# Performance work log

Measured on AMD Instinct MI355X. Metric: run time of the kernel, lower is better.

## Reference

```python
import jax, jax.numpy as jnp
import numpy as np

B, D, N, H, K = 8192, 1024, 4096, 8, 4
T, DECAY, STEPS = 100.0, 0.001, 3


def setup_inputs() -> dict:
    key = jax.random.key(0)
    ks = jax.random.split(key, 16)
    rn = lambda k, sh, s=0.02: jax.random.normal(k, sh, jnp.float32) * s
    return {
        'query': jax.random.normal(ks[0], (B, D), jnp.float32),
        'wm': jax.random.normal(ks[1], (B, D), jnp.float32),
        'keys': jax.random.normal(ks[2], (N, D), jnp.float32) * 0.1,
        'values': jax.random.normal(ks[3], (N, D), jnp.float32) * 0.1,
        'last_access': jax.random.uniform(ks[4], (N,), jnp.float32) * T,
        'importance': jnp.ones((N,), jnp.float32),
        'consolid': jnp.ones((N,), jnp.float32),
        'emo_tags': jax.random.uniform(ks[5], (N, 8), jnp.float32),
        'active': jnp.ones((N,), jnp.float32),
        'in_proj_w': rn(ks[6], (3 * D, D)), 'in_proj_b': jnp.zeros((3 * D,), jnp.float32),
        'out_w': rn(ks[7], (D, D)), 'out_b': jnp.zeros((D,), jnp.float32),
        'msg_w1': rn(ks[8], (D, 2 * D)), 'msg_b1': jnp.zeros((D,), jnp.float32),
        'msg_ln_g': jnp.ones((D,), jnp.float32), 'msg_ln_b': jnp.zeros((D,), jnp.float32),
        'msg_w2': rn(ks[9], (D, D)), 'msg_b2': jnp.zeros((D,), jnp.float32),
        'gru_wih': rn(ks[10], (3 * D, D)), 'gru_whh': rn(ks[11], (3 * D, D)),
        'gru_bih': jnp.zeros((3 * D,), jnp.float32), 'gru_bhh': jnp.zeros((3 * D,), jnp.float32),
        'rsn_w1': rn(ks[12], (D, D)), 'rsn_b1': jnp.zeros((D,), jnp.float32),
        'rsn_ln_g': jnp.ones((D,), jnp.float32), 'rsn_ln_b': jnp.zeros((D,), jnp.float32),
        'rsn_w2': rn(ks[13], (D, D)), 'rsn_b2': jnp.zeros((D,), jnp.float32),
        'top_k': K,
    }


def _ln(x, g, b):
    m = x.mean(-1, keepdims=True)
    v = ((x - m) ** 2).mean(-1, keepdims=True)
    return (x - m) / jnp.sqrt(v + 1e-5) * g + b


def reference(query, wm, keys, values, last_access, importance, consolid, emo_tags, active,
              in_proj_w, in_proj_b, out_w, out_b,
              msg_w1, msg_b1, msg_ln_g, msg_ln_b, msg_w2, msg_b2,
              gru_wih, gru_whh, gru_bih, gru_bhh,
              rsn_w1, rsn_b1, rsn_ln_g, rsn_ln_b, rsn_w2, rsn_b2, top_k):
    sg = jax.lax.stop_gradient
    # --- schema retrieve: cosine sim + forgetting-decay + boosts + topk softmax gather ---
    qn = query / jnp.maximum(jnp.linalg.norm(query, axis=-1, keepdims=True), 1e-8)
    kn = keys / jnp.maximum(jnp.linalg.norm(keys, axis=-1, keepdims=True), 1e-8)
    sims = qn @ kn.T  # [B, N]
    forget = sg(jnp.exp(-DECAY * (T - last_access)))
    boost = sg(emo_tags.sum(-1) * 0.1 + importance * 0.2 + jnp.log1p(consolid) * 0.1)
    scores = (sims * forget + boost) * sg(active)
    top_s, top_i = jax.lax.top_k(scores, top_k)  # [B, K]
    w = jax.nn.softmax(top_s, axis=-1)
    schema = jnp.einsum('bk,bkd->bd', w, values[top_i])  # [B, D]

    # --- GraphReasoner: 3 steps of 2-token MHA + msg_net + GRUCell ---
    dh = D // H
    scale = 1.0 / np.sqrt(dh).astype(np.float32)

    def mha(x):  # x [B, 2, D]
        qkv = x @ in_proj_w.T + in_proj_b
        q, k, v = jnp.split(qkv, 3, axis=-1)
        q = q.reshape(-1, 2, H, dh); k = k.reshape(-1, 2, H, dh); v = v.reshape(-1, 2, H, dh)
        a = jax.nn.softmax(jnp.einsum('bqhd,bkhd->bhqk', q, k) * scale, axis=-1)
        o = jnp.einsum('bhqk,bkhd->bqhd', a, v).reshape(-1, 2, D)
        return o @ out_w.T + out_b

    def gru(x, h):
        gi = x @ gru_wih.T + gru_bih
        gh = h @ gru_whh.T + gru_bhh
        ir, iz, inn = jnp.split(gi, 3, axis=-1)
        hr, hz, hn = jnp.split(gh, 3, axis=-1)
        r = jax.nn.sigmoid(ir + hr)
        z = jax.nn.sigmoid(iz + hz)
        n = jnp.tanh(inn + r * hn)
        return (1.0 - z) * n + z * h

    state = wm
    for _ in range(STEPS):
        ctx = jnp.stack([state, schema], axis=1)  # [B, 2, D]
        att = mha(ctx)
        combined = jnp.concatenate([att[:, 0], att[:, 1]], axis=-1)  # [B, 2D]
        msg = jax.nn.relu(_ln(combined @ msg_w1.T + msg_b1, msg_ln_g, msg_ln_b)) @ msg_w2.T + msg_b2
        state = gru(msg, state)
    out = jax.nn.relu(_ln(state @ rsn_w1.T + rsn_b1, rsn_ln_g, rsn_ln_b)) @ rsn_w2.T + rsn_b2
    return out
```

## Files before the change

kernel.cpp:

```cpp
#include <hip/hip_runtime.h>
#include <cstdint>
#include <cstddef>

typedef __attribute__((ext_vector_type(8))) short short8;
typedef __attribute__((ext_vector_type(4))) float f32x4;
typedef __attribute__((ext_vector_type(4))) unsigned short us4;

#define DEVINL static __device__ __forceinline__

DEVINL float bf2f(unsigned short u){
  union { unsigned uu; float f; } v; v.uu = ((unsigned)u) << 16; return v.f;
}
DEVINL unsigned short f2bf(float f){
  unsigned u = __float_as_uint(f);
  u += 0x7fffu + ((u >> 16) & 1u);
  return (unsigned short)(u >> 16);
}

DEVINL bool tk_better(float av, int ai, float bv, int bi){
  return (av > bv) || (av == bv && ai < bi);
}
DEVINL void tk_cmpex(float& va, int& ia, float& vb, int& ib){
  if (!tk_better(va, ia, vb, ib)){
    float tv = va; va = vb; vb = tv;
    int t = ia; ia = ib; ib = t;
  }
}
DEVINL void tk_sort4(float* v, int* id){
  tk_cmpex(v[0], id[0], v[1], id[1]);
  tk_cmpex(v[2], id[2], v[3], id[3]);
  tk_cmpex(v[0], id[0], v[2], id[2]);
  tk_cmpex(v[1], id[1], v[3], id[3]);
  tk_cmpex(v[1], id[1], v[2], id[2]);
}
DEVINL void tk_bmerge(float* v, int* id, const float* pv, const int* pi){
  #pragma unroll
  for (int i = 0; i < 4; ++i){
    bool ta = tk_better(v[i], id[i], pv[3 - i], pi[3 - i]);
    v[i]  = ta ? v[i]  : pv[3 - i];
    id[i] = ta ? id[i] : pi[3 - i];
  }
  tk_cmpex(v[0], id[0], v[2], id[2]);
  tk_cmpex(v[1], id[1], v[3], id[3]);
  tk_cmpex(v[0], id[0], v[1], id[1]);
  tk_cmpex(v[2], id[2], v[3], id[3]);
}

__global__ void k_diag(float* out, float v){ out[0] = v; }

__global__ __launch_bounds__(256) void k_cast_bf16(const float* __restrict__ x,
                                                   unsigned short* __restrict__ y, int n4){
  int stride = gridDim.x * blockDim.x;
  for (int i = blockIdx.x * blockDim.x + threadIdx.x; i < n4; i += stride){
    float4 v = ((const float4*)x)[i];
    us4 o; o[0] = f2bf(v.x); o[1] = f2bf(v.y); o[2] = f2bf(v.z); o[3] = f2bf(v.w);
    ((us4*)y)[i] = o;
  }
}

__global__ __launch_bounds__(256) void k_prep_keys(const float* __restrict__ keys,
    const float* __restrict__ last_access, const float* __restrict__ importance,
    const float* __restrict__ consolid, const float* __restrict__ emo,
    const float* __restrict__ active, float* __restrict__ ascale, float* __restrict__ bbias){
  int wave = threadIdx.x >> 6, lane = threadIdx.x & 63;
  int n = blockIdx.x * 4 + wave;
  const float* kr = keys + (size_t)n * 1024;
  float s = 0.f;
  #pragma unroll
  for (int j = 0; j < 4; ++j){
    float4 v = ((const float4*)kr)[j * 64 + lane];
    s += v.x*v.x + v.y*v.y + v.z*v.z + v.w*v.w;
  }
  #pragma unroll
  for (int m = 32; m >= 1; m >>= 1) s += __shfl_xor(s, m);
  if (lane == 0){
    float norm = fmaxf(sqrtf(s), 1e-8f);
    float forget = expf(-0.001f * (100.0f - last_access[n]));
    float bo = 0.f;
    #pragma unroll
    for (int j = 0; j < 8; ++j) bo += emo[n * 8 + j];
    bo = bo * 0.1f + importance[n] * 0.2f + log1pf(consolid[n]) * 0.1f;
    float a = active[n];
    ascale[n] = forget * a / norm;
    bbias[n]  = bo * a;
  }
}

__global__ __launch_bounds__(256) void k_qnorm(const float* __restrict__ q, float* __restrict__ qinv){
  int wave = threadIdx.x >> 6, lane = threadIdx.x & 63;
  int b = blockIdx.x * 4 + wave;
  const float* qr = q + (size_t)b * 1024;
  float s = 0.f;
  #pragma unroll
  for (int j = 0; j < 4; ++j){
    float4 v = ((const float4*)qr)[j * 64 + lane];
    s += v.x*v.x + v.y*v.y + v.z*v.z + v.w*v.w;
  }
  #pragma unroll
  for (int m = 32; m >= 1; m >>= 1) s += __shfl_xor(s, m);
  if (lane == 0) qinv[b] = 1.0f / fmaxf(sqrtf(s), 1e-8f);
}

__global__ __launch_bounds__(256) void k_split(const float* __restrict__ X,
    const float* __restrict__ rscale, unsigned short* __restrict__ Hi,
    unsigned short* __restrict__ Lo){
  const int row = blockIdx.x;
  const float sc = rscale ? rscale[row] : 1.0f;
  const int d = threadIdx.x * 4;
  float4 v = *(const float4*)(X + (size_t)row * 1024 + d);
  float xs[4] = {v.x * sc, v.y * sc, v.z * sc, v.w * sc};
  us4 h, l;
  #pragma unroll
  for (int j = 0; j < 4; ++j){
    unsigned short hb = f2bf(xs[j]);
    h[j] = hb;
    l[j] = f2bf(xs[j] - bf2f(hb));
  }
  *(us4*)(Hi + (size_t)row * 1024 + d) = h;
  *(us4*)(Lo + (size_t)row * 1024 + d) = l;
}

__global__ __launch_bounds__(256) void k_scores_mfma(
    const unsigned short* __restrict__ Qhi, const unsigned short* __restrict__ Qlo,
    const unsigned short* __restrict__ Khi, const unsigned short* __restrict__ Klo,
    const float* __restrict__ ascale, const float* __restrict__ bbias,
    float* __restrict__ candV, int* __restrict__ candI){
  __shared__ __align__(16) unsigned short AsH[128 * 32];
  __shared__ __align__(16) unsigned short AsL[128 * 32];
  __shared__ __align__(16) unsigned short BsH[128 * 32];
  __shared__ __align__(16) unsigned short BsL[128 * 32];
  const int tid = threadIdx.x;
  const int wave = tid >> 6, lane = tid & 63;
  const int tM = blockIdx.x, tN = blockIdx.y;
  const int wm_ = wave >> 1, wn_ = wave & 1;
  f32x4 acc[4][4] = {};
  const unsigned short* AH = Qhi + (size_t)tM * 128 * 1024;
  const unsigned short* AL = Qlo + (size_t)tM * 128 * 1024;
  const unsigned short* BH = Khi + (size_t)tN * 128 * 1024;
  const unsigned short* BL = Klo + (size_t)tN * 128 * 1024;
  const int lrow = lane & 15, lk = (lane >> 4) * 8;
  for (int k0 = 0; k0 < 1024; k0 += 32){
    __syncthreads();
    #pragma unroll
    for (int j = 0; j < 2; ++j){
      int c = wave * 128 + j * 64 + lane;
      int row = c >> 2, cp = c & 3;
      size_t go = (size_t)row * 1024 + k0 + cp * 8;
      int lo_ = (wave * 2 + j) * 512;
      __builtin_amdgcn_global_load_lds((const __attribute__((address_space(1))) void*)(AH + go),
          (__attribute__((address_space(3))) void*)(AsH + lo_), 16, 0, 0);
      __builtin_amdgcn_global_load_lds((const __attribute__((address_space(1))) void*)(AL + go),
          (__attribute__((address_space(3))) void*)(AsL + lo_), 16, 0, 0);
      __builtin_amdgcn_global_load_lds((const __attribute__((address_space(1))) void*)(BH + go),
          (__attribute__((address_space(3))) void*)(BsH + lo_), 16, 0, 0);
      __builtin_amdgcn_global_load_lds((const __attribute__((address_space(1))) void*)(BL + go),
          (__attribute__((address_space(3))) void*)(BsL + lo_), 16, 0, 0);
    }
    __syncthreads();
    short8 ah[4], al[4], bh[4], bl[4];
    #pragma unroll
    for (int mi = 0; mi < 4; ++mi){
      int ro = (wm_ * 64 + mi * 16 + lrow) * 32 + lk;
      ah[mi] = *(const short8*)(AsH + ro);
      al[mi] = *(const short8*)(AsL + ro);
    }
    #pragma unroll
    for (int ni = 0; ni < 4; ++ni){
      int ro = (wn_ * 64 + ni * 16 + lrow) * 32 + lk;
      bh[ni] = *(const short8*)(BsH + ro);
      bl[ni] = *(const short8*)(BsL + ro);
    }
    #pragma unroll
    for (int mi = 0; mi < 4; ++mi)
      #pragma unroll
      for (int ni = 0; ni < 4; ++ni){
        acc[mi][ni] = __builtin_amdgcn_mfma_f32_16x16x32_bf16(ah[mi], bh[ni], acc[mi][ni], 0, 0, 0);
        acc[mi][ni] = __builtin_amdgcn_mfma_f32_16x16x32_bf16(ah[mi], bl[ni], acc[mi][ni], 0, 0, 0);
        acc[mi][ni] = __builtin_amdgcn_mfma_f32_16x16x32_bf16(al[mi], bh[ni], acc[mi][ni], 0, 0, 0);
      }
  }
  const int lc = lane & 15;
  float as_[4], bb_[4]; int cid[4];
  #pragma unroll
  for (int ni = 0; ni < 4; ++ni){
    cid[ni] = tN * 128 + wn_ * 64 + ni * 16 + lc;
    as_[ni] = ascale[cid[ni]];
    bb_[ni] = bbias[cid[ni]];
  }
  #pragma unroll
  for (int mi = 0; mi < 4; ++mi){
    #pragma unroll
    for (int r = 0; r < 4; ++r){
      float v[4]; int id[4];
      #pragma unroll
      for (int ni = 0; ni < 4; ++ni){
        v[ni]  = acc[mi][ni][r] * as_[ni] + bb_[ni];
        id[ni] = cid[ni];
      }
      tk_sort4(v, id);
      #pragma unroll
      for (int mask = 1; mask <= 8; mask <<= 1){
        float pv[4]; int pi_[4];
        #pragma unroll
        for (int j = 0; j < 4; ++j){
          pv[j]  = __shfl_xor(v[j], mask);
          pi_[j] = __shfl_xor(id[j], mask);
        }
        tk_bmerge(v, id, pv, pi_);
      }
      if (lc == 0){
        int row = tM * 128 + wm_ * 64 + mi * 16 + (lane >> 4) * 4 + r;
        size_t cb = (size_t)row * 256 + tN * 8 + wn_ * 4;
        #pragma unroll
        for (int j = 0; j < 4; ++j){ candV[cb + j] = v[j]; candI[cb + j] = id[j]; }
      }
    }
  }
}

__global__ __launch_bounds__(256) void k_topk_merge(const float* __restrict__ candV,
    const int* __restrict__ candI, const float* __restrict__ V,
    unsigned short* __restrict__ schema_bf){
  const int row = blockIdx.x, tid = threadIdx.x;
  const int wave = tid >> 6, lane = tid & 63;
  float v[4]; int id[4];
  v[0] = candV[(size_t)row * 256 + tid];
  id[0] = candI[(size_t)row * 256 + tid];
  #pragma unroll
  for (int j = 1; j < 4; ++j){ v[j] = -3.4e38f; id[j] = 0x7fffffff; }
  #pragma unroll
  for (int mask = 1; mask <= 32; mask <<= 1){
    float pv[4]; int pi_[4];
    #pragma unroll
    for (int j = 0; j < 4; ++j){
      pv[j]  = __shfl_xor(v[j], mask);
      pi_[j] = __shfl_xor(id[j], mask);
    }
    tk_bmerge(v, id, pv, pi_);
  }
  __shared__ float wv[4][4]; __shared__ int wi[4][4];
  if (lane == 0){
    #pragma unroll
    for (int j = 0; j < 4; ++j){ wv[wave][j] = v[j]; wi[wave][j] = id[j]; }
  }
  __syncthreads();
  __shared__ float w_sh[4]; __shared__ int i_sh[4];
  if (tid == 0){
    float fv[4]; int fi[4];
    #pragma unroll
    for (int j = 0; j < 4; ++j){ fv[j] = wv[0][j]; fi[j] = wi[0][j]; }
    #pragma unroll
    for (int w = 1; w < 4; ++w){
      float pv[4]; int pi_[4];
      #pragma unroll
      for (int j = 0; j < 4; ++j){ pv[j] = wv[w][j]; pi_[j] = wi[w][j]; }
      tk_bmerge(fv, fi, pv, pi_);
    }
    float m = fv[0];
    float e0 = expf(fv[0] - m), e1 = expf(fv[1] - m), e2 = expf(fv[2] - m), e3 = expf(fv[3] - m);
    float inv = 1.f / (e0 + e1 + e2 + e3);
    w_sh[0] = e0 * inv; w_sh[1] = e1 * inv; w_sh[2] = e2 * inv; w_sh[3] = e3 * inv;
    i_sh[0] = fi[0]; i_sh[1] = fi[1]; i_sh[2] = fi[2]; i_sh[3] = fi[3];
  }
  __syncthreads();
  float w0 = w_sh[0], w1 = w_sh[1], w2 = w_sh[2], w3 = w_sh[3];
  const float* v0 = V + (size_t)i_sh[0] * 1024;
  const float* v1 = V + (size_t)i_sh[1] * 1024;
  const float* v2 = V + (size_t)i_sh[2] * 1024;
  const float* v3 = V + (size_t)i_sh[3] * 1024;
  int d = tid * 4;
  float4 a = *(const float4*)(v0 + d);
  float4 b4 = *(const float4*)(v1 + d);
  float4 c = *(const float4*)(v2 + d);
  float4 e = *(const float4*)(v3 + d);
  us4 o;
  o[0] = f2bf(w0*a.x + w1*b4.x + w2*c.x + w3*e.x);
  o[1] = f2bf(w0*a.y + w1*b4.y + w2*c.y + w3*e.y);
  o[2] = f2bf(w0*a.z + w1*b4.z + w2*c.z + w3*e.z);
  o[3] = f2bf(w0*a.w + w1*b4.w + w2*c.w + w3*e.w);
  *(us4*)(schema_bf + (size_t)row * 1024 + d) = o;
}

__global__ __launch_bounds__(256) void k_initstate(const float* __restrict__ wm,
    float* __restrict__ st, unsigned short* __restrict__ stbf){
  size_t i = ((size_t)blockIdx.x * 256 + threadIdx.x) * 4;
  float4 v = *(const float4*)(wm + i);
  *(float4*)(st + i) = v;
  us4 o; o[0] = f2bf(v.x); o[1] = f2bf(v.y); o[2] = f2bf(v.z); o[3] = f2bf(v.w);
  *(us4*)(stbf + i) = o;
}

template<int OUT_BF16>
__global__ __launch_bounds__(256) void k_gemm(const unsigned short* __restrict__ A,
    const unsigned short* __restrict__ W, const float* __restrict__ bias,
    void* __restrict__ C, int M, int N, int K){
  __shared__ __align__(16) unsigned short As[128 * 32];
  __shared__ __align__(16) unsigned short Ws[128 * 32];
  const int tid = threadIdx.x;
  const int wave = tid >> 6, lane = tid & 63;
  const int tM = blockIdx.x, tN = blockIdx.y;
  const int wm_ = wave >> 1, wn_ = wave & 1;
  f32x4 acc[4][4] = {};
  const unsigned short* Abase = A + (size_t)tM * 128 * K;
  const unsigned short* Wbase = W + (size_t)tN * 128 * K;
  const int lrow = lane & 15, lk = (lane >> 4) * 8;
  for (int k0 = 0; k0 < K; k0 += 32){
    __syncthreads();
    #pragma unroll
    for (int j = 0; j < 2; ++j){
      int c = wave * 128 + j * 64 + lane;
      int row = c >> 2, cp = c & 3;
      const unsigned short* ga = Abase + (size_t)row * K + k0 + cp * 8;
      const unsigned short* gw = Wbase + (size_t)row * K + k0 + cp * 8;
      __builtin_amdgcn_global_load_lds((const __attribute__((address_space(1))) void*)ga,
          (__attribute__((address_space(3))) void*)(As + (wave * 2 + j) * 512), 16, 0, 0);
      __builtin_amdgcn_global_load_lds((const __attribute__((address_space(1))) void*)gw,
          (__attribute__((address_space(3))) void*)(Ws + (wave * 2 + j) * 512), 16, 0, 0);
    }
    __syncthreads();
    short8 af[4], bfr[4];
    #pragma unroll
    for (int mi = 0; mi < 4; ++mi)
      af[mi] = *(const short8*)(As + (wm_ * 64 + mi * 16 + lrow) * 32 + lk);
    #pragma unroll
    for (int ni = 0; ni < 4; ++ni)
      bfr[ni] = *(const short8*)(Ws + (wn_ * 64 + ni * 16 + lrow) * 32 + lk);
    #pragma unroll
    for (int mi = 0; mi < 4; ++mi)
      #pragma unroll
      for (int ni = 0; ni < 4; ++ni)
        acc[mi][ni] = __builtin_amdgcn_mfma_f32_16x16x32_bf16(af[mi], bfr[ni], acc[mi][ni], 0, 0, 0);
  }
  const int lc = lane & 15, lr = (lane >> 4) * 4;
  #pragma unroll
  for (int ni = 0; ni < 4; ++ni){
    int col = tN * 128 + wn_ * 64 + ni * 16 + lc;
    float bb = bias ? bias[col] : 0.f;
    #pragma unroll
    for (int mi = 0; mi < 4; ++mi){
      int rowb = tM * 128 + wm_ * 64 + mi * 16 + lr;
      #pragma unroll
      for (int r = 0; r < 4; ++r){
        float vv = acc[mi][ni][r] + bb;
        size_t off = (size_t)(rowb + r) * N + col;
        if (OUT_BF16) ((unsigned short*)C)[off] = f2bf(vv);
        else ((float*)C)[off] = vv;
      }
    }
  }
}

__global__ __launch_bounds__(256) void k_attn(const unsigned short* __restrict__ qkvS,
    const unsigned short* __restrict__ qkvM, unsigned short* __restrict__ o){
  const int b = blockIdx.x, tid = threadIdx.x;
  const int l = tid & 31;
  const int e = (tid >> 5) * 128 + l * 4;
  const unsigned short* ps = qkvS + (size_t)b * 3072;
  const unsigned short* pm = qkvM + (size_t)b * 3072;
  float q0[4], kk0[4], v0[4], q1[4], kk1[4], v1[4];
  us4 t;
  t = *(const us4*)(ps + e);        for (int j = 0; j < 4; ++j) q0[j]  = bf2f(t[j]);
  t = *(const us4*)(ps + 1024 + e); for (int j = 0; j < 4; ++j) kk0[j] = bf2f(t[j]);
  t = *(const us4*)(ps + 2048 + e); for (int j = 0; j < 4; ++j) v0[j]  = bf2f(t[j]);
  t = *(const us4*)(pm + e);        for (int j = 0; j < 4; ++j) q1[j]  = bf2f(t[j]);
  t = *(const us4*)(pm + 1024 + e); for (int j = 0; j < 4; ++j) kk1[j] = bf2f(t[j]);
  t = *(const us4*)(pm + 2048 + e); for (int j = 0; j < 4; ++j) v1[j]  = bf2f(t[j]);
  float s00 = 0.f, s01 = 0.f, s10 = 0.f, s11 = 0.f;
  #pragma unroll
  for (int j = 0; j < 4; ++j){
    s00 += q0[j] * kk0[j]; s01 += q0[j] * kk1[j];
    s10 += q1[j] * kk0[j]; s11 += q1[j] * kk1[j];
  }
  #pragma unroll
  for (int m = 16; m >= 1; m >>= 1){
    s00 += __shfl_xor(s00, m); s01 += __shfl_xor(s01, m);
    s10 += __shfl_xor(s10, m); s11 += __shfl_xor(s11, m);
  }
  const float sc = 0.08838834764831845f;
  s00 *= sc; s01 *= sc; s10 *= sc; s11 *= sc;
  float m0 = fmaxf(s00, s01), m1 = fmaxf(s10, s11);
  float e00 = expf(s00 - m0), e01 = expf(s01 - m0);
  float e10 = expf(s10 - m1), e11 = expf(s11 - m1);
  float i0 = 1.f / (e00 + e01), i1 = 1.f / (e10 + e11);
  float w00 = e00 * i0, w01 = e01 * i0, w10 = e10 * i1, w11 = e11 * i1;
  us4 o0, o1;
  #pragma unroll
  for (int j = 0; j < 4; ++j){
    o0[j] = f2bf(w00 * v0[j] + w01 * v1[j]);
    o1[j] = f2bf(w10 * v0[j] + w11 * v1[j]);
  }
  *(us4*)(o + ((size_t)b * 2) * 1024 + e)     = o0;
  *(us4*)(o + ((size_t)b * 2 + 1) * 1024 + e) = o1;
}

__global__ __launch_bounds__(256) void k_ln_relu(const float* __restrict__ X,
    const float* __restrict__ g, const float* __restrict__ bta, unsigned short* __restrict__ Y){
  const int row = blockIdx.x, tid = threadIdx.x;
  const float* x = X + (size_t)row * 1024;
  const int d = tid * 4;
  float4 v = *(const float4*)(x + d);
  float s1 = v.x + v.y + v.z + v.w;
  float s2 = v.x*v.x + v.y*v.y + v.z*v.z + v.w*v.w;
  #pragma unroll
  for (int m = 32; m >= 1; m >>= 1){ s1 += __shfl_xor(s1, m); s2 += __shfl_xor(s2, m); }
  __shared__ float a1[4], a2[4];
  int wave = tid >> 6, lane = tid & 63;
  if (lane == 0){ a1[wave] = s1; a2[wave] = s2; }
  __syncthreads();
  s1 = a1[0] + a1[1] + a1[2] + a1[3];
  s2 = a2[0] + a2[1] + a2[2] + a2[3];
  float mean = s1 * (1.f / 1024.f);
  float var  = s2 * (1.f / 1024.f) - mean * mean;
  float rstd = rsqrtf(var + 1e-5f);
  float4 gg = *(const float4*)(g + d);
  float4 bb = *(const float4*)(bta + d);
  us4 o;
  o[0] = f2bf(fmaxf((v.x - mean) * rstd * gg.x + bb.x, 0.f));
  o[1] = f2bf(fmaxf((v.y - mean) * rstd * gg.y + bb.y, 0.f));
  o[2] = f2bf(fmaxf((v.z - mean) * rstd * gg.z + bb.z, 0.f));
  o[3] = f2bf(fmaxf((v.w - mean) * rstd * gg.w + bb.w, 0.f));
  *(us4*)(Y + (size_t)row * 1024 + d) = o;
}

__global__ __launch_bounds__(256) void k_gru(const unsigned short* __restrict__ gi,
    const unsigned short* __restrict__ gh, const float* __restrict__ h,
    float* __restrict__ hn, unsigned short* __restrict__ hnbf){
  const int b = blockIdx.x;
  const int d = threadIdx.x * 4;
  const unsigned short* pi = gi + (size_t)b * 3072;
  const unsigned short* ph = gh + (size_t)b * 3072;
  us4 t;
  float ir[4], iz[4], in_[4], hr[4], hz[4], hnn[4];
  t = *(const us4*)(pi + d);        for (int j = 0; j < 4; ++j) ir[j]  = bf2f(t[j]);
  t = *(const us4*)(pi + 1024 + d); for (int j = 0; j < 4; ++j) iz[j]  = bf2f(t[j]);
  t = *(const us4*)(pi + 2048 + d); for (int j = 0; j < 4; ++j) in_[j] = bf2f(t[j]);
  t = *(const us4*)(ph + d);        for (int j = 0; j < 4; ++j) hr[j]  = bf2f(t[j]);
  t = *(const us4*)(ph + 1024 + d); for (int j = 0; j < 4; ++j) hz[j]  = bf2f(t[j]);
  t = *(const us4*)(ph + 2048 + d); for (int j = 0; j < 4; ++j) hnn[j] = bf2f(t[j]);
  float4 hv = *(const float4*)(h + (size_t)b * 1024 + d);
  float hvv[4] = {hv.x, hv.y, hv.z, hv.w};
  float ov[4]; us4 ob;
  #pragma unroll
  for (int j = 0; j < 4; ++j){
    float r = 1.f / (1.f + expf(-(ir[j] + hr[j])));
    float z = 1.f / (1.f + expf(-(iz[j] + hz[j])));
    float n = tanhf(in_[j] + r * hnn[j]);
    float o = (1.f - z) * n + z * hvv[j];
    ov[j] = o; ob[j] = f2bf(o);
  }
  float4 of; of.x = ov[0]; of.y = ov[1]; of.z = ov[2]; of.w = ov[3];
  *(float4*)(hn + (size_t)b * 1024 + d) = of;
  *(us4*)(hnbf + (size_t)b * 1024 + d) = ob;
}

extern "C" void kernel_launch(void* const* d_in, const int* in_sizes, int n_in,
                              void* d_out, int out_size, void* d_ws, size_t ws_size,
                              hipStream_t stream) {
  (void)in_sizes; (void)n_in; (void)out_size;
  const float* query       = (const float*)d_in[0];
  const float* wm          = (const float*)d_in[1];
  const float* keys        = (const float*)d_in[2];
  const float* values      = (const float*)d_in[3];
  const float* last_access = (const float*)d_in[4];
  const float* importance  = (const float*)d_in[5];
  const float* consolid    = (const float*)d_in[6];
  const float* emo         = (const float*)d_in[7];
  const float* active      = (const float*)d_in[8];
  const float* in_proj_w   = (const float*)d_in[9];
  const float* in_proj_b   = (const float*)d_in[10];
  const float* out_w       = (const float*)d_in[11];
  const float* out_b       = (const float*)d_in[12];
  const float* msg_w1      = (const float*)d_in[13];
  const float* msg_b1      = (const float*)d_in[14];
  const float* msg_ln_g    = (const float*)d_in[15];
  const float* msg_ln_b    = (const float*)d_in[16];
  const float* msg_w2      = (const float*)d_in[17];
  const float* msg_b2      = (const float*)d_in[18];
  const float* gru_wih     = (const float*)d_in[19];
  const float* gru_whh     = (const float*)d_in[20];
  const float* gru_bih     = (const float*)d_in[21];
  const float* gru_bhh     = (const float*)d_in[22];
  const float* rsn_w1      = (const float*)d_in[23];
  const float* rsn_b1      = (const float*)d_in[24];
  const float* rsn_ln_g    = (const float*)d_in[25];
  const float* rsn_ln_b    = (const float*)d_in[26];
  const float* rsn_w2      = (const float*)d_in[27];
  const float* rsn_b2      = (const float*)d_in[28];
  float* out = (float*)d_out;

  size_t off = 0;
  char* base = (char*)d_ws;
  auto carve = [&](size_t bytes) -> char* {
    char* p = base + off;
    off += (bytes + 255) & ~(size_t)255;
    return p;
  };
  float* ascale = (float*)carve(4096*4);
  float* bbias  = (float*)carve(4096*4);
  float* qinv   = (float*)carve(8192*4);
  unsigned short* wb_inproj = (unsigned short*)carve((size_t)3072*1024*2);
  unsigned short* wb_outw   = (unsigned short*)carve((size_t)1024*1024*2);
  unsigned short* wb_msgw1  = (unsigned short*)carve((size_t)1024*2048*2);
  unsigned short* wb_msgw2  = (unsigned short*)carve((size_t)1024*1024*2);
  unsigned short* wb_gwih   = (unsigned short*)carve((size_t)3072*1024*2);
  unsigned short* wb_gwhh   = (unsigned short*)carve((size_t)3072*1024*2);
  unsigned short* wb_rw1    = (unsigned short*)carve((size_t)1024*1024*2);
  unsigned short* wb_rw2    = (unsigned short*)carve((size_t)1024*1024*2);
  unsigned short* schema_bf = (unsigned short*)carve((size_t)8192*1024*2);
  float*          state_f   = (float*)carve((size_t)8192*1024*4);
  unsigned short* state_bf  = (unsigned short*)carve((size_t)8192*1024*2);
  unsigned short* qkvM      = (unsigned short*)carve((size_t)8192*3072*2);
  unsigned short* bufP      = (unsigned short*)carve((size_t)8192*3072*2);
  unsigned short* bufQ      = (unsigned short*)carve((size_t)8192*3072*2);

  if (off > ws_size){
    k_diag<<<1, 1, 0, stream>>>(out, (float)(ws_size >> 20));
    return;
  }

  unsigned short* Qhi = qkvM;
  unsigned short* Qlo = Qhi + (size_t)8192*1024;
  unsigned short* Khi = Qlo + (size_t)8192*1024;
  unsigned short* Klo = Khi + (size_t)4096*1024;
  float* candV = (float*)bufP;
  int*   candI = (int*)((char*)bufP + (size_t)8192*256*4);

  unsigned short* qkvS   = bufP;
  unsigned short* obuf   = bufQ;
  unsigned short* attbuf = bufP;
  float*          preln  = (float*)bufQ;
  unsigned short* h1buf  = bufP;
  unsigned short* msgbuf = bufQ;
  unsigned short* gibuf  = bufP;
  unsigned short* ghbuf  = bufQ;

  auto cast = [&](const float* src, unsigned short* dst, int n){
    k_cast_bf16<<<1024, 256, 0, stream>>>(src, dst, n / 4);
  };
  cast(in_proj_w, wb_inproj, 3072*1024);
  cast(out_w,   wb_outw,  1024*1024);
  cast(msg_w1,  wb_msgw1, 1024*2048);
  cast(msg_w2,  wb_msgw2, 1024*1024);
  cast(gru_wih, wb_gwih,  3072*1024);
  cast(gru_whh, wb_gwhh,  3072*1024);
  cast(rsn_w1,  wb_rw1,   1024*1024);
  cast(rsn_w2,  wb_rw2,   1024*1024);

  k_qnorm<<<2048, 256, 0, stream>>>(query, qinv);
  k_prep_keys<<<1024, 256, 0, stream>>>(keys, last_access, importance, consolid, emo, active, ascale, bbias);
  k_split<<<8192, 256, 0, stream>>>(query, qinv, Qhi, Qlo);
  k_split<<<4096, 256, 0, stream>>>(keys, nullptr, Khi, Klo);
  k_scores_mfma<<<dim3(64, 32), 256, 0, stream>>>(Qhi, Qlo, Khi, Klo, ascale, bbias, candV, candI);
  k_topk_merge<<<8192, 256, 0, stream>>>(candV, candI, values, schema_bf);

  k_initstate<<<8192, 256, 0, stream>>>(wm, state_f, state_bf);
  k_gemm<1><<<dim3(64, 24), 256, 0, stream>>>(schema_bf, wb_inproj, in_proj_b, qkvM, 8192, 3072, 1024);
  for (int s = 0; s < 3; ++s){
    k_gemm<1><<<dim3(64, 24), 256, 0, stream>>>(state_bf, wb_inproj, in_proj_b, qkvS, 8192, 3072, 1024);
    k_attn<<<8192, 256, 0, stream>>>(qkvS, qkvM, obuf);
    k_gemm<1><<<dim3(128, 8), 256, 0, stream>>>(obuf, wb_outw, out_b, attbuf, 16384, 1024, 1024);
    k_gemm<0><<<dim3(64, 8), 256, 0, stream>>>(attbuf, wb_msgw1, msg_b1, preln, 8192, 1024, 2048);
    k_ln_relu<<<8192, 256, 0, stream>>>(preln, msg_ln_g, msg_ln_b, h1buf);
    k_gemm<1><<<dim3(64, 8), 256, 0, stream>>>(h1buf, wb_msgw2, msg_b2, msgbuf, 8192, 1024, 1024);
    k_gemm<1><<<dim3(64, 24), 256, 0, stream>>>(msgbuf, wb_gwih, gru_bih, gibuf, 8192, 3072, 1024);
    k_gemm<1><<<dim3(64, 24), 256, 0, stream>>>(state_bf, wb_gwhh, gru_bhh, ghbuf, 8192, 3072, 1024);
    k_gru<<<8192, 256, 0, stream>>>(gibuf, ghbuf, state_f, state_f, state_bf);
  }
  k_gemm<0><<<dim3(64, 8), 256, 0, stream>>>(state_bf, wb_rw1, rsn_b1, (float*)bufP, 8192, 1024, 1024);
  k_ln_relu<<<8192, 256, 0, stream>>>((float*)bufP, rsn_ln_g, rsn_ln_b, bufQ);
  k_gemm<0><<<dim3(64, 8), 256, 0, stream>>>(bufQ, wb_rw2, rsn_b2, out, 8192, 1024, 1024);
}
```

Measured before the change: 1.805 ms.

## Fold out_proj into msg_w1 and msg_w2 into GRU input weights

Measured after the change: 1.647 ms. 8.8% less time.

```diff
diff --git a/kernel.cpp b/kernel.cpp
--- a/kernel.cpp
+++ b/kernel.cpp
@@ -56,6 +56,44 @@
     us4 o; o[0] = f2bf(v.x); o[1] = f2bf(v.y); o[2] = f2bf(v.z); o[3] = f2bf(v.w);
     ((us4*)y)[i] = o;
   }
+}
+
+__global__ __launch_bounds__(256) void k_tcast(const float* __restrict__ in,
+    unsigned short* __restrict__ outT, int R, int C){
+  __shared__ float t[32][33];
+  const int bc = blockIdx.x * 32, br = blockIdx.y * 32;
+  const int lx = threadIdx.x & 31, ly = threadIdx.x >> 5;
+  #pragma unroll
+  for (int i = 0; i < 32; i += 8)
+    t[ly + i][lx] = in[(size_t)(br + ly + i) * C + bc + lx];
+  __syncthreads();
+  #pragma unroll
+  for (int i = 0; i < 32; i += 8)
+    outT[(size_t)(bc + ly + i) * R + br + lx] = f2bf(t[lx][ly + i]);
+}
+
+__global__ __launch_bounds__(256) void k_bias_pre(const float* __restrict__ w1,
+    const float* __restrict__ outb, const float* __restrict__ b1, float* __restrict__ bc){
+  int wave = threadIdx.x >> 6, lane = threadIdx.x & 63;
+  int j = blockIdx.x * 4 + wave;
+  float s = 0.f;
+  for (int m = lane; m < 2048; m += 64)
+    s += w1[(size_t)j * 2048 + m] * outb[m & 1023];
+  #pragma unroll
+  for (int m = 32; m >= 1; m >>= 1) s += __shfl_xor(s, m);
+  if (lane == 0) bc[j] = s + b1[j];
+}
+
+__global__ __launch_bounds__(256) void k_bias_gi(const float* __restrict__ wih,
+    const float* __restrict__ b2, const float* __restrict__ bih, float* __restrict__ bc){
+  int wave = threadIdx.x >> 6, lane = threadIdx.x & 63;
+  int n = blockIdx.x * 4 + wave;
+  float s = 0.f;
+  for (int m = lane; m < 1024; m += 64)
+    s += wih[(size_t)n * 1024 + m] * b2[m];
+  #pragma unroll
+  for (int m = 32; m >= 1; m >>= 1) s += __shfl_xor(s, m);
+  if (lane == 0) bc[n] = s + bih[n];
 }
 
 __global__ __launch_bounds__(256) void k_prep_keys(const float* __restrict__ keys,
@@ -293,7 +331,7 @@
 template<int OUT_BF16>
 __global__ __launch_bounds__(256) void k_gemm(const unsigned short* __restrict__ A,
     const unsigned short* __restrict__ W, const float* __restrict__ bias,
-    void* __restrict__ C, int M, int N, int K){
+    void* __restrict__ C, int M, int N, int K, int lda, int ldc){
   __shared__ __align__(16) unsigned short As[128 * 32];
   __shared__ __align__(16) unsigned short Ws[128 * 32];
   const int tid = threadIdx.x;
@@ -301,7 +339,7 @@
   const int tM = blockIdx.x, tN = blockIdx.y;
   const int wm_ = wave >> 1, wn_ = wave & 1;
   f32x4 acc[4][4] = {};
-  const unsigned short* Abase = A + (size_t)tM * 128 * K;
+  const unsigned short* Abase = A + (size_t)tM * 128 * lda;
   const unsigned short* Wbase = W + (size_t)tN * 128 * K;
   const int lrow = lane & 15, lk = (lane >> 4) * 8;
   for (int k0 = 0; k0 < K; k0 += 32){
@@ -310,7 +348,7 @@
     for (int j = 0; j < 2; ++j){
       int c = wave * 128 + j * 64 + lane;
       int row = c >> 2, cp = c & 3;
-      const unsigned short* ga = Abase + (size_t)row * K + k0 + cp * 8;
+      const unsigned short* ga = Abase + (size_t)row * lda + k0 + cp * 8;
       const unsigned short* gw = Wbase + (size_t)row * K + k0 + cp * 8;
       __builtin_amdgcn_global_load_lds((const __attribute__((address_space(1))) void*)ga,
           (__attribute__((address_space(3))) void*)(As + (wave * 2 + j) * 512), 16, 0, 0);
@@ -342,7 +380,7 @@
       #pragma unroll
       for (int r = 0; r < 4; ++r){
         float vv = acc[mi][ni][r] + bb;
-        size_t off = (size_t)(rowb + r) * N + col;
+        size_t off = (size_t)(rowb + r) * ldc + col;
         if (OUT_BF16) ((unsigned short*)C)[off] = f2bf(vv);
         else ((float*)C)[off] = vv;
       }
@@ -351,7 +389,7 @@
 }
 
 __global__ __launch_bounds__(256) void k_attn(const unsigned short* __restrict__ qkvS,
-    const unsigned short* __restrict__ qkvM, unsigned short* __restrict__ o){
+    const unsigned short* __restrict__ qkvM, unsigned short* __restrict__ catt){
   const int b = blockIdx.x, tid = threadIdx.x;
   const int l = tid & 31;
   const int e = (tid >> 5) * 128 + l * 4;
@@ -389,8 +427,8 @@
     o0[j] = f2bf(w00 * v0[j] + w01 * v1[j]);
     o1[j] = f2bf(w10 * v0[j] + w11 * v1[j]);
   }
-  *(us4*)(o + ((size_t)b * 2) * 1024 + e)     = o0;
-  *(us4*)(o + ((size_t)b * 2 + 1) * 1024 + e) = o1;
+  *(us4*)(catt + (size_t)b * 2048 + e)        = o0;
+  *(us4*)(catt + (size_t)b * 2048 + 1024 + e) = o1;
 }
 
 __global__ __launch_bounds__(256) void k_ln_relu(const float* __restrict__ X,
@@ -498,14 +536,14 @@
   float* ascale = (float*)carve(4096*4);
   float* bbias  = (float*)carve(4096*4);
   float* qinv   = (float*)carve(8192*4);
+  float* bc_pre = (float*)carve(1024*4);
+  float* bc_gi  = (float*)carve(3072*4);
   unsigned short* wb_inproj = (unsigned short*)carve((size_t)3072*1024*2);
-  unsigned short* wb_outw   = (unsigned short*)carve((size_t)1024*1024*2);
-  unsigned short* wb_msgw1  = (unsigned short*)carve((size_t)1024*2048*2);
-  unsigned short* wb_msgw2  = (unsigned short*)carve((size_t)1024*1024*2);
-  unsigned short* wb_gwih   = (unsigned short*)carve((size_t)3072*1024*2);
   unsigned short* wb_gwhh   = (unsigned short*)carve((size_t)3072*1024*2);
   unsigned short* wb_rw1    = (unsigned short*)carve((size_t)1024*1024*2);
   unsigned short* wb_rw2    = (unsigned short*)carve((size_t)1024*1024*2);
+  unsigned short* wb_Wab    = (unsigned short*)carve((size_t)1024*2048*2);
+  unsigned short* wb_Wc     = (unsigned short*)carve((size_t)3072*1024*2);
   unsigned short* schema_bf = (unsigned short*)carve((size_t)8192*1024*2);
   float*          state_f   = (float*)carve((size_t)8192*1024*4);
   unsigned short* state_bf  = (unsigned short*)carve((size_t)8192*1024*2);
@@ -518,6 +556,11 @@
     return;
   }
 
+  unsigned short* tmp_w1bf  = bufQ;
+  unsigned short* tmp_outwT = bufQ + (size_t)1024*2048;
+  unsigned short* tmp_w2T   = tmp_outwT + (size_t)1024*1024;
+  unsigned short* tmp_wihbf = tmp_w2T + (size_t)1024*1024;
+
   unsigned short* Qhi = qkvM;
   unsigned short* Qlo = Qhi + (size_t)8192*1024;
   unsigned short* Khi = Qlo + (size_t)8192*1024;
@@ -525,26 +568,29 @@
   float* candV = (float*)bufP;
   int*   candI = (int*)((char*)bufP + (size_t)8192*256*4);
 
-  unsigned short* qkvS   = bufP;
-  unsigned short* obuf   = bufQ;
-  unsigned short* attbuf = bufP;
-  float*          preln  = (float*)bufQ;
-  unsigned short* h1buf  = bufP;
-  unsigned short* msgbuf = bufQ;
-  unsigned short* gibuf  = bufP;
-  unsigned short* ghbuf  = bufQ;
+  unsigned short* qkvS  = bufP;
+  unsigned short* catt  = bufQ;
+  float*          preln = (float*)bufP;
+  unsigned short* h1buf = bufQ;
+  unsigned short* gibuf = bufP;
+  unsigned short* ghbuf = bufQ;
 
   auto cast = [&](const float* src, unsigned short* dst, int n){
     k_cast_bf16<<<1024, 256, 0, stream>>>(src, dst, n / 4);
   };
   cast(in_proj_w, wb_inproj, 3072*1024);
-  cast(out_w,   wb_outw,  1024*1024);
-  cast(msg_w1,  wb_msgw1, 1024*2048);
-  cast(msg_w2,  wb_msgw2, 1024*1024);
-  cast(gru_wih, wb_gwih,  3072*1024);
-  cast(gru_whh, wb_gwhh,  3072*1024);
-  cast(rsn_w1,  wb_rw1,   1024*1024);
-  cast(rsn_w2,  wb_rw2,   1024*1024);
+  cast(gru_whh,   wb_gwhh,   3072*1024);
+  cast(rsn_w1,    wb_rw1,    1024*1024);
+  cast(rsn_w2,    wb_rw2,    1024*1024);
+  cast(msg_w1,    tmp_w1bf,  1024*2048);
+  cast(gru_wih,   tmp_wihbf, 3072*1024);
+  k_tcast<<<dim3(32, 32), 256, 0, stream>>>(out_w,  tmp_outwT, 1024, 1024);
+  k_tcast<<<dim3(32, 32), 256, 0, stream>>>(msg_w2, tmp_w2T,   1024, 1024);
+  k_bias_pre<<<256, 256, 0, stream>>>(msg_w1, out_b, msg_b1, bc_pre);
+  k_bias_gi<<<768, 256, 0, stream>>>(gru_wih, msg_b2, gru_bih, bc_gi);
+  k_gemm<1><<<dim3(8, 8), 256, 0, stream>>>(tmp_w1bf,        tmp_outwT, nullptr, wb_Wab,        1024, 1024, 1024, 2048, 2048);
+  k_gemm<1><<<dim3(8, 8), 256, 0, stream>>>(tmp_w1bf + 1024, tmp_outwT, nullptr, wb_Wab + 1024, 1024, 1024, 1024, 2048, 2048);
+  k_gemm<1><<<dim3(24, 8), 256, 0, stream>>>(tmp_wihbf, tmp_w2T, nullptr, wb_Wc, 3072, 1024, 1024, 1024, 1024);
 
   k_qnorm<<<2048, 256, 0, stream>>>(query, qinv);
   k_prep_keys<<<1024, 256, 0, stream>>>(keys, last_access, importance, consolid, emo, active, ascale, bbias);
@@ -554,19 +600,17 @@
   k_topk_merge<<<8192, 256, 0, stream>>>(candV, candI, values, schema_bf);
 
   k_initstate<<<8192, 256, 0, stream>>>(wm, state_f, state_bf);
-  k_gemm<1><<<dim3(64, 24), 256, 0, stream>>>(schema_bf, wb_inproj, in_proj_b, qkvM, 8192, 3072, 1024);
+  k_gemm<1><<<dim3(64, 24), 256, 0, stream>>>(schema_bf, wb_inproj, in_proj_b, qkvM, 8192, 3072, 1024, 1024, 3072);
   for (int s = 0; s < 3; ++s){
-    k_gemm<1><<<dim3(64, 24), 256, 0, stream>>>(state_bf, wb_inproj, in_proj_b, qkvS, 8192, 3072, 1024);
-    k_attn<<<8192, 256, 0, stream>>>(qkvS, qkvM, obuf);
-    k_gemm<1><<<dim3(128, 8), 256, 0, stream>>>(obuf, wb_outw, out_b, attbuf, 16384, 1024, 1024);
-    k_gemm<0><<<dim3(64, 8), 256, 0, stream>>>(attbuf, wb_msgw1, msg_b1, preln, 8192, 1024, 2048);
+    k_gemm<1><<<dim3(64, 24), 256, 0, stream>>>(state_bf, wb_inproj, in_proj_b, qkvS, 8192, 3072, 1024, 1024, 3072);
+    k_attn<<<8192, 256, 0, stream>>>(qkvS, qkvM, catt);
+    k_gemm<0><<<dim3(64, 8), 256, 0, stream>>>(catt, wb_Wab, bc_pre, preln, 8192, 1024, 2048, 2048, 1024);
     k_ln_relu<<<8192, 256, 0, stream>>>(preln, msg_ln_g, msg_ln_b, h1buf);
-    k_gemm<1><<<dim3(64, 8), 256, 0, stream>>>(h1buf, wb_msgw2, msg_b2, msgbuf, 8192, 1024, 1024);
-    k_gemm<1><<<dim3(64, 24), 256, 0, stream>>>(msgbuf, wb_gwih, gru_bih, gibuf, 8192, 3072, 1024);
-    k_gemm<1><<<dim3(64, 24), 256, 0, stream>>>(state_bf, wb_gwhh, gru_bhh, ghbuf, 8192, 3072, 1024);
+    k_gemm<1><<<dim3(64, 24), 256, 0, stream>>>(h1buf, wb_Wc, bc_gi, gibuf, 8192, 3072, 1024, 1024, 3072);
+    k_gemm<1><<<dim3(64, 24), 256, 0, stream>>>(state_bf, wb_gwhh, gru_bhh, ghbuf, 8192, 3072, 1024, 1024, 3072);
     k_gru<<<8192, 256, 0, stream>>>(gibuf, ghbuf, state_f, state_f, state_bf);
   }
-  k_gemm<0><<<dim3(64, 8), 256, 0, stream>>>(state_bf, wb_rw1, rsn_b1, (float*)bufP, 8192, 1024, 1024);
+  k_gemm<0><<<dim3(64, 8), 256, 0, stream>>>(state_bf, wb_rw1, rsn_b1, (float*)bufP, 8192, 1024, 1024, 1024, 1024);
   k_ln_relu<<<8192, 256, 0, stream>>>((float*)bufP, rsn_ln_g, rsn_ln_b, bufQ);
-  k_gemm<0><<<dim3(64, 8), 256, 0, stream>>>(bufQ, wb_rw2, rsn_b2, out, 8192, 1024, 1024);
-}
+  k_gemm<0><<<dim3(64, 8), 256, 0, stream>>>(bufQ, wb_rw2, rsn_b2, out, 8192, 1024, 1024, 1024, 1024);
+}
```
